# Optimization experiments

Measured on AMD Instinct MI355X. Metric: run time of the kernel, lower is better.

## Reference

```python
import jax, jax.numpy as jnp
import numpy as np

N = 100000   # nodes
E = 1600000  # edges
C = 128      # hidden_channels
L = 3        # num_layers
V = 128      # embedding vocab


def setup_inputs() -> dict:
    key = jax.random.key(0)
    ks = jax.random.split(key, 10)
    s = 1.0 / np.sqrt(C)
    return {
        "x_idx": jax.random.randint(ks[0], (N,), 0, V),
        "edge_index": jax.random.randint(ks[1], (2, E), 0, N),
        "edge_weight": jax.random.uniform(ks[2], (E,), dtype=jnp.float32),
        "emb": jax.random.normal(ks[3], (V, C), dtype=jnp.float32),
        "conv_w": jax.random.uniform(ks[4], (L, C, C), minval=-s, maxval=s, dtype=jnp.float32),
        "conv_b": jnp.zeros((L, C), dtype=jnp.float32),
        "lin1_w": jax.random.uniform(ks[5], (C, C), minval=-s, maxval=s, dtype=jnp.float32),
        "lin1_b": jnp.zeros((C,), dtype=jnp.float32),
        "lin2_w": jax.random.uniform(ks[6], (C, 2), minval=-s, maxval=s, dtype=jnp.float32),
        "lin2_b": jnp.zeros((2,), dtype=jnp.float32),
    }


def reference(x_idx, edge_index, edge_weight, emb, conv_w, conv_b,
              lin1_w, lin1_b, lin2_w, lin2_b):
    # GCNConv (PyG): add self-loops (weight 1), symmetric normalization
    row, col = edge_index[0], edge_index[1]
    loop = jnp.arange(N)
    r = jnp.concatenate([row, loop])
    c = jnp.concatenate([col, loop])
    w = jnp.concatenate([edge_weight, jnp.ones((N,), edge_weight.dtype)])
    deg = jax.ops.segment_sum(w, c, num_segments=N)            # [N]
    dinv = jnp.where(deg > 0, jax.lax.rsqrt(deg), 0.0)
    norm = dinv[r] * w * dinv[c]                               # [E+N]

    x = emb[x_idx]                                             # [N, C]
    for i in range(L):
        xw = x @ conv_w[i]                                     # [N, C]
        # message: norm * xw[src], aggregate at dst
        x = jax.ops.segment_sum(norm[:, None] * xw[r], c, num_segments=N) + conv_b[i]
        if i < L - 1:
            x = jax.nn.relu(x)  # dropout is identity in eval mode

    x = jax.nn.relu(x @ lin1_w + lin1_b)
    return x @ lin2_w + lin2_b                                 # [N, 2]
```

## Files before the change

kernel.cpp:

```cpp
#include <hip/hip_runtime.h>
#include <hip/hip_fp16.h>

#define NN 100000
#define NE 1600000
#define CC 128
#define NBIN 782
#define BPW 128
#define MAXB 2560
#define NHB 256
#define EPB 6250

typedef _Float16 f16x8 __attribute__((ext_vector_type(8)));
typedef float    f32x4 __attribute__((ext_vector_type(4)));

__global__ __launch_bounds__(256) void k_prep0(const int* __restrict__ ei,
                                               const float* __restrict__ conv_w,
                                               const float* __restrict__ lin1_w,
                                               const float* __restrict__ emb,
                                               int* __restrict__ hist,
                                               _Float16* __restrict__ wt,
                                               __half2* __restrict__ ewh,
                                               int* __restrict__ counter) {
    int blk = blockIdx.x;
    if (blk < NHB) {
        __shared__ int h[NBIN];
        for (int i = threadIdx.x; i < NBIN; i += 256) h[i] = 0;
        __syncthreads();
        int base = blk * EPB;
        for (int i = threadIdx.x; i < EPB; i += 256) {
            int d = ei[NE + base + i];
            atomicAdd(&h[d >> 7], 1);
        }
        __syncthreads();
        for (int i = threadIdx.x; i < NBIN; i += 256)
            hist[blk * NBIN + i] = h[i];
        if (blk == 0 && threadIdx.x == 0) *counter = 0;
    } else if (blk < NHB + 192) {
        int t = (blk - NHB) * 256 + threadIdx.x;
        int l = t >> 14, r = t & 16383;
        int j = r >> 7, k = r & 127;
        const float* src = (l < 2) ? (conv_w + (l + 1) * 16384) : lin1_w;
        wt[l * 16384 + j * 128 + k] = (_Float16)src[k * 128 + j];
    } else {
        int t = (blk - NHB - 192) * 256 + threadIdx.x;
        int i = t >> 6, jp = t & 63, j0 = jp * 2;
        float a0 = 0.f, a1 = 0.f;
        for (int k = 0; k < 128; k++) {
            float e = emb[i * 128 + k];
            a0 = fmaf(e, conv_w[k * 128 + j0], a0);
            a1 = fmaf(e, conv_w[k * 128 + j0 + 1], a1);
        }
        ewh[t] = __floats2half2_rn(a0, a1);
    }
}

__global__ __launch_bounds__(256) void k_scanA(const int* __restrict__ hist,
                                               int* __restrict__ blockBase,
                                               int* __restrict__ binTotal,
                                               int* __restrict__ binStart,
                                               int* __restrict__ counter) {
    __shared__ int s[256];
    __shared__ bool amLast;
    int bin = blockIdx.x, t = threadIdx.x;
    int v = hist[t * NBIN + bin];
    s[t] = v; __syncthreads();
    for (int off = 1; off < 256; off <<= 1) {
        int x = (t >= off) ? s[t - off] : 0;
        __syncthreads();
        s[t] += x;
        __syncthreads();
    }
    blockBase[t * NBIN + bin] = s[t] - v;
    if (t == 255) {
        binTotal[bin] = s[255];
        __threadfence();
        int d = atomicAdd(counter, 1);
        amLast = (d == NBIN - 1);
    }
    __syncthreads();
    if (!amLast) return;
    int loc[4];
    int sum = 0;
#pragma unroll
    for (int j = 0; j < 4; j++) {
        int idx = t * 4 + j;
        int x = (idx < NBIN) ? atomicAdd(&binTotal[idx], 0) : 0;
        loc[j] = sum; sum += x;
    }
    __syncthreads();
    s[t] = sum; __syncthreads();
    for (int off = 1; off < 256; off <<= 1) {
        int x = (t >= off) ? s[t - off] : 0;
        __syncthreads();
        s[t] += x;
        __syncthreads();
    }
    int base = s[t] - sum;
#pragma unroll
    for (int j = 0; j < 4; j++) {
        int idx = t * 4 + j;
        if (idx < NBIN) binStart[idx] = base + loc[j];
    }
    if (t == 255) binStart[NBIN] = s[255];
}

__global__ __launch_bounds__(256) void k_pass2(const int* __restrict__ ei,
                                               const float* __restrict__ ew,
                                               const int* __restrict__ binStart,
                                               const int* __restrict__ blockBase,
                                               int2* __restrict__ pay,
                                               unsigned char* __restrict__ key) {
    __shared__ int cur[NBIN];
    int blk = blockIdx.x;
    for (int i = threadIdx.x; i < NBIN; i += 256)
        cur[i] = binStart[i] + blockBase[blk * NBIN + i];
    __syncthreads();
    int base = blk * EPB;
    for (int i = threadIdx.x; i < EPB; i += 256) {
        int e = base + i;
        int d = ei[NE + e];
        int src = ei[e];
        float w = ew[e];
        int pos = atomicAdd(&cur[d >> 7], 1);
        pay[pos] = make_int2(src, __float_as_int(w));
        key[pos] = (unsigned char)(d & 127);
    }
}

__global__ __launch_bounds__(256) void k_pass3(const int* __restrict__ binStart,
                                               const int2* __restrict__ pay,
                                               const unsigned char* __restrict__ key,
                                               int2* __restrict__ csr,
                                               int* __restrict__ rowptr,
                                               float* __restrict__ dinv) {
    __shared__ int2 sp[MAXB];
    __shared__ unsigned char sk[MAXB];
    __shared__ int hist[BPW], excl[BPW], cur[BPW];
    __shared__ float degw[BPW];
    int b = blockIdx.x, t = threadIdx.x;
    int s0 = binStart[b], s1 = binStart[b + 1];
    int n = s1 - s0;
    if (t < BPW) { hist[t] = 0; degw[t] = 0.f; }
    __syncthreads();
    for (int i = t; i < n; i += 256) {
        int2 p = pay[s0 + i];
        unsigned char k = key[s0 + i];
        sp[i] = p; sk[i] = k;
        atomicAdd(&hist[k], 1);
    }
    __syncthreads();
    if (t < BPW) excl[t] = hist[t];
    __syncthreads();
    for (int off = 1; off < BPW; off <<= 1) {
        int x = (t < BPW && t >= off) ? excl[t - off] : 0;
        __syncthreads();
        if (t < BPW) excl[t] += x;
        __syncthreads();
    }
    if (t < BPW) {
        int ex = excl[t] - hist[t];
        excl[t] = ex;
        cur[t] = ex;
    }
    __syncthreads();
    int node0 = b * BPW;
    if (t < BPW && node0 + t < NN) rowptr[node0 + t] = s0 + excl[t];
    if (b == NBIN - 1 && t == 0) rowptr[NN] = NE;
    for (int i = t; i < n; i += 256) {
        int2 p = sp[i];
        unsigned char k = sk[i];
        int pos = atomicAdd(&cur[k], 1);
        csr[s0 + pos] = p;
        atomicAdd(&degw[k], __int_as_float(p.y));
    }
    __syncthreads();
    if (t < BPW && node0 + t < NN) dinv[node0 + t] = rsqrtf(1.f + degw[t]);
}

__global__ void k_mkcsr0(const int2* __restrict__ csr, const int* __restrict__ xidx,
                         const float* __restrict__ dinv, int2* __restrict__ csr0) {
    int e = blockIdx.x * 256 + threadIdx.x;
    if (e < NE) {
        int2 c = csr[e];
        csr0[e] = make_int2(xidx[c.x],
                            __float_as_int(__int_as_float(c.y) * dinv[c.x]));
    }
}

template <int SELF_TABLE, int RELU>
__device__ __forceinline__ void agg_core(const _Float16* __restrict__ src16,
                                         const int2* __restrict__ csr,
                                         const int* __restrict__ rowptr,
                                         const int* __restrict__ xidx,
                                         const float* __restrict__ dinv,
                                         const float* __restrict__ bias,
                                         _Float16* __restrict__ xout) {
    int wave = threadIdx.x >> 6, lane = threadIdx.x & 63;
    int g = lane >> 4, sub = lane & 15;
    int v = blockIdx.x * 4 + wave;
    if (v >= NN) return;
    int beg = rowptr[v], end = rowptr[v + 1];
    const unsigned long long* csr64 =
        reinterpret_cast<const unsigned long long*>(csr);

    auto lde = [&](int idx, float& w) -> f16x8 {
        unsigned long long raw = __builtin_nontemporal_load(csr64 + idx);
        int s = (int)(unsigned)(raw & 0xffffffffu);
        w = __int_as_float((int)(raw >> 32));
        return *reinterpret_cast<const f16x8*>(&src16[(size_t)s * 128 + sub * 8]);
    };

    float acc[8];
#pragma unroll
    for (int i = 0; i < 8; i++) acc[i] = 0.f;

    int e = beg;
    while (e + 16 <= end) {
        float w0, w1, w2, w3;
        f16x8 t0 = lde(e + g, w0);
        f16x8 t1 = lde(e + 4 + g, w1);
        f16x8 t2 = lde(e + 8 + g, w2);
        f16x8 t3 = lde(e + 12 + g, w3);
#pragma unroll
        for (int i = 0; i < 8; i++) acc[i] = fmaf(w0, (float)t0[i], acc[i]);
#pragma unroll
        for (int i = 0; i < 8; i++) acc[i] = fmaf(w1, (float)t1[i], acc[i]);
#pragma unroll
        for (int i = 0; i < 8; i++) acc[i] = fmaf(w2, (float)t2[i], acc[i]);
#pragma unroll
        for (int i = 0; i < 8; i++) acc[i] = fmaf(w3, (float)t3[i], acc[i]);
        e += 16;
    }
    if (e + 8 <= end) {
        float w0, w1;
        f16x8 t0 = lde(e + g, w0);
        f16x8 t1 = lde(e + 4 + g, w1);
#pragma unroll
        for (int i = 0; i < 8; i++) acc[i] = fmaf(w0, (float)t0[i], acc[i]);
#pragma unroll
        for (int i = 0; i < 8; i++) acc[i] = fmaf(w1, (float)t1[i], acc[i]);
        e += 8;
    }
    for (; e < end; e += 4) {
        int idx = e + g;
        bool ok = idx < end;
        float w0;
        f16x8 t0 = lde(ok ? idx : beg, w0);
        if (!ok) w0 = 0.f;
#pragma unroll
        for (int i = 0; i < 8; i++) acc[i] = fmaf(w0, (float)t0[i], acc[i]);
    }

#pragma unroll
    for (int i = 0; i < 8; i++) {
        acc[i] += __shfl_down(acc[i], 32);
        acc[i] += __shfl_down(acc[i], 16);
    }
    if (g == 0) {
        float dv = dinv[v];
        size_t selfoff = SELF_TABLE ? (size_t)xidx[v] * 128 : (size_t)v * 128;
        f16x8 sf = *reinterpret_cast<const f16x8*>(&src16[selfoff + sub * 8]);
        float4 b0 = reinterpret_cast<const float4*>(bias)[sub * 2];
        float4 b1 = reinterpret_cast<const float4*>(bias)[sub * 2 + 1];
        float bb[8] = {b0.x, b0.y, b0.z, b0.w, b1.x, b1.y, b1.z, b1.w};
        f16x8 o;
#pragma unroll
        for (int i = 0; i < 8; i++) {
            float self = SELF_TABLE ? dv * (float)sf[i] : (float)sf[i];
            float r = fmaf(dv, acc[i] + self, bb[i]);
            if (RELU) r = fmaxf(r, 0.f);
            o[i] = (_Float16)r;
        }
        __builtin_nontemporal_store(
            o, reinterpret_cast<f16x8*>(&xout[(size_t)v * 128 + sub * 8]));
    }
}

__global__ void k_agg0(const int2* __restrict__ csr0, const int* __restrict__ rowptr,
                       const int* __restrict__ xidx, const float* __restrict__ dinv,
                       const _Float16* __restrict__ ewh, const float* __restrict__ bias,
                       _Float16* __restrict__ xout) {
    agg_core<1, 1>(ewh, csr0, rowptr, xidx, dinv, bias, xout);
}

__global__ void k_agg_r(const _Float16* __restrict__ y, const int* __restrict__ rowptr,
                        const int2* __restrict__ csr, const float* __restrict__ dinv,
                        const float* __restrict__ bias, _Float16* __restrict__ xout) {
    agg_core<0, 1>(y, csr, rowptr, nullptr, dinv, bias, xout);
}

__global__ void k_agg_n(const _Float16* __restrict__ y, const int* __restrict__ rowptr,
                        const int2* __restrict__ csr, const float* __restrict__ dinv,
                        const float* __restrict__ bias, _Float16* __restrict__ xout) {
    agg_core<0, 0>(y, csr, rowptr, nullptr, dinv, bias, xout);
}

template <int MODE>
__global__ __launch_bounds__(256) void k_mgemm(const _Float16* __restrict__ A,
                                               const _Float16* __restrict__ Wt,
                                               const float* __restrict__ dinv,
                                               const float* __restrict__ bias,
                                               _Float16* __restrict__ yout,
                                               const float* __restrict__ w2,
                                               const float* __restrict__ b2,
                                               float* __restrict__ outf) {
    int wid = threadIdx.x >> 6, lane = threadIdx.x & 63;
    int lc = lane & 15, lg = lane >> 4;
    int arow = blockIdx.x * 64 + wid * 16 + lc;
    bool rok = arow < NN;

    f32x4 acc[8];
#pragma unroll
    for (int j = 0; j < 8; j++) acc[j] = (f32x4){0.f, 0.f, 0.f, 0.f};

#pragma unroll
    for (int kc = 0; kc < 4; kc++) {
        int k0 = kc * 32 + lg * 8;
        f16x8 a = {0, 0, 0, 0, 0, 0, 0, 0};
        if (rok) a = *reinterpret_cast<const f16x8*>(&A[arow * 128 + k0]);
#pragma unroll
        for (int j = 0; j < 8; j++) {
            f16x8 b = *reinterpret_cast<const f16x8*>(&Wt[(j * 16 + lc) * 128 + k0]);
            acc[j] = __builtin_amdgcn_mfma_f32_16x16x32_f16(a, b, acc[j], 0, 0, 0);
        }
    }

    int orow0 = blockIdx.x * 64 + wid * 16 + lg * 4;
    if (MODE == 0) {
        float dv[4];
#pragma unroll
        for (int r = 0; r < 4; r++)
            dv[r] = (orow0 + r < NN) ? dinv[orow0 + r] : 0.f;
#pragma unroll
        for (int j = 0; j < 8; j++) {
#pragma unroll
            for (int r = 0; r < 4; r++) {
                int orow = orow0 + r;
                if (orow < NN)
                    yout[orow * 128 + j * 16 + lc] = (_Float16)(dv[r] * acc[j][r]);
            }
        }
    } else {
        float bj[8], w0j[8], w1j[8];
#pragma unroll
        for (int j = 0; j < 8; j++) {
            int c = j * 16 + lc;
            bj[j] = bias[c];
            w0j[j] = w2[c * 2 + 0];
            w1j[j] = w2[c * 2 + 1];
        }
        float bb0 = b2[0], bb1 = b2[1];
#pragma unroll
        for (int r = 0; r < 4; r++) {
            float p0 = 0.f, p1 = 0.f;
#pragma unroll
            for (int j = 0; j < 8; j++) {
                float h = fmaxf(acc[j][r] + bj[j], 0.f);
                p0 = fmaf(h, w0j[j], p0);
                p1 = fmaf(h, w1j[j], p1);
            }
#pragma unroll
            for (int m = 1; m < 16; m <<= 1) {
                p0 += __shfl_xor(p0, m);
                p1 += __shfl_xor(p1, m);
            }
            int orow = orow0 + r;
            if (lc == 0 && orow < NN)
                *reinterpret_cast<float2*>(&outf[orow * 2]) =
                    make_float2(p0 + bb0, p1 + bb1);
        }
    }
}

extern "C" void kernel_launch(void* const* d_in, const int* in_sizes, int n_in,
                              void* d_out, int out_size, void* d_ws, size_t ws_size,
                              hipStream_t stream) {
    const int*   x_idx  = (const int*)d_in[0];
    const int*   ei     = (const int*)d_in[1];
    const float* ew     = (const float*)d_in[2];
    const float* emb    = (const float*)d_in[3];
    const float* conv_w = (const float*)d_in[4];
    const float* conv_b = (const float*)d_in[5];
    const float* lin1_w = (const float*)d_in[6];
    const float* lin1_b = (const float*)d_in[7];
    const float* lin2_w = (const float*)d_in[8];
    const float* lin2_b = (const float*)d_in[9];
    float* out = (float*)d_out;

    char* ws = (char*)d_ws;
    size_t off = 0;
    auto alloc = [&](size_t bytes) -> void* {
        void* p = ws + off;
        off += (bytes + 255) & ~(size_t)255;
        return p;
    };
    float*         dinv      = (float*)alloc(NN * 4);
    int*           rowptr    = (int*)alloc((NN + 1) * 4);
    int*           hist      = (int*)alloc((size_t)NHB * NBIN * 4);
    int*           blockBase = (int*)alloc((size_t)NHB * NBIN * 4);
    int*           binTotal  = (int*)alloc(NBIN * 4);
    int*           binStart  = (int*)alloc((NBIN + 1) * 4);
    int*           counter   = (int*)alloc(256);
    int2*          pay       = (int2*)alloc((size_t)NE * 8);
    unsigned char* key       = (unsigned char*)alloc(NE);
    int2*          csr       = (int2*)alloc((size_t)NE * 8);
    int2*          csr0      = (int2*)alloc((size_t)NE * 8);
    _Float16*      ewh       = (_Float16*)alloc(128 * 128 * 2);
    _Float16*      wt        = (_Float16*)alloc(3 * 128 * 128 * 2);
    _Float16*      xbuf      = (_Float16*)alloc((size_t)NN * CC * 2);
    _Float16*      ybuf      = (_Float16*)alloc((size_t)NN * CC * 2);
    (void)ws_size;

    const int NBe = (NE + 255) / 256;
    const int NBg = (NN + 63) / 64;

    k_prep0<<<NHB + 192 + 32, 256, 0, stream>>>(ei, conv_w, lin1_w, emb,
                                                hist, wt, (__half2*)ewh, counter);
    k_scanA<<<NBIN, 256, 0, stream>>>(hist, blockBase, binTotal, binStart, counter);
    k_pass2<<<NHB, 256, 0, stream>>>(ei, ew, binStart, blockBase, pay, key);
    k_pass3<<<NBIN, 256, 0, stream>>>(binStart, pay, key, csr, rowptr, dinv);
    k_mkcsr0<<<NBe, 256, 0, stream>>>(csr, x_idx, dinv, csr0);

    k_agg0<<<NN / 4, 256, 0, stream>>>(csr0, rowptr, x_idx, dinv, ewh,
                                       conv_b + 0 * CC, xbuf);
    k_mgemm<0><<<NBg, 256, 0, stream>>>(xbuf, wt + 0 * 16384, dinv, nullptr, ybuf,
                                        nullptr, nullptr, nullptr);
    k_agg_r<<<NN / 4, 256, 0, stream>>>(ybuf, rowptr, csr, dinv, conv_b + 1 * CC, xbuf);
    k_mgemm<0><<<NBg, 256, 0, stream>>>(xbuf, wt + 1 * 16384, dinv, nullptr, ybuf,
                                        nullptr, nullptr, nullptr);
    k_agg_n<<<NN / 4, 256, 0, stream>>>(ybuf, rowptr, csr, dinv, conv_b + 2 * CC, xbuf);
    k_mgemm<1><<<NBg, 256, 0, stream>>>(xbuf, wt + 2 * 16384, dinv, lin1_b, nullptr,
                                        lin2_w, lin2_b, out);
}
```

Baseline: 426.2 us.

## Fuse neighbor aggregation with following MFMA GEMM through shared memory

Merges each aggregation kernel with the following dense MFMA transform. Each block aggregates 64 nodes into an LDS tile, then multiplies that tile by the weights directly, so the intermediate x buffer never goes to global memory and three launches disappear. The trade-off is that each wave now walks 16 nodes one after another instead of one node per wave, with a grid about 16x smaller. The edge loop is also reduced from 16- to 8-edge unrolling with ordinary rather than nontemporal loads, which cuts memory-level parallelism in a gather-bound phase.

```diff
diff --git a/kernel.cpp b/kernel.cpp
--- a/kernel.cpp
+++ b/kernel.cpp
@@ -187,146 +187,98 @@
     }
 }
 
-template <int SELF_TABLE, int RELU>
-__device__ __forceinline__ void agg_core(const _Float16* __restrict__ src16,
-                                         const int2* __restrict__ csr,
-                                         const int* __restrict__ rowptr,
-                                         const int* __restrict__ xidx,
-                                         const float* __restrict__ dinv,
-                                         const float* __restrict__ bias,
-                                         _Float16* __restrict__ xout) {
-    int wave = threadIdx.x >> 6, lane = threadIdx.x & 63;
-    int g = lane >> 4, sub = lane & 15;
-    int v = blockIdx.x * 4 + wave;
-    if (v >= NN) return;
-    int beg = rowptr[v], end = rowptr[v + 1];
-    const unsigned long long* csr64 =
-        reinterpret_cast<const unsigned long long*>(csr);
-
-    auto lde = [&](int idx, float& w) -> f16x8 {
-        unsigned long long raw = __builtin_nontemporal_load(csr64 + idx);
-        int s = (int)(unsigned)(raw & 0xffffffffu);
-        w = __int_as_float((int)(raw >> 32));
-        return *reinterpret_cast<const f16x8*>(&src16[(size_t)s * 128 + sub * 8]);
-    };
-
-    float acc[8];
-#pragma unroll
-    for (int i = 0; i < 8; i++) acc[i] = 0.f;
-
-    int e = beg;
-    while (e + 16 <= end) {
-        float w0, w1, w2, w3;
-        f16x8 t0 = lde(e + g, w0);
-        f16x8 t1 = lde(e + 4 + g, w1);
-        f16x8 t2 = lde(e + 8 + g, w2);
-        f16x8 t3 = lde(e + 12 + g, w3);
-#pragma unroll
-        for (int i = 0; i < 8; i++) acc[i] = fmaf(w0, (float)t0[i], acc[i]);
-#pragma unroll
-        for (int i = 0; i < 8; i++) acc[i] = fmaf(w1, (float)t1[i], acc[i]);
-#pragma unroll
-        for (int i = 0; i < 8; i++) acc[i] = fmaf(w2, (float)t2[i], acc[i]);
-#pragma unroll
-        for (int i = 0; i < 8; i++) acc[i] = fmaf(w3, (float)t3[i], acc[i]);
-        e += 16;
-    }
-    if (e + 8 <= end) {
-        float w0, w1;
-        f16x8 t0 = lde(e + g, w0);
-        f16x8 t1 = lde(e + 4 + g, w1);
-#pragma unroll
-        for (int i = 0; i < 8; i++) acc[i] = fmaf(w0, (float)t0[i], acc[i]);
-#pragma unroll
-        for (int i = 0; i < 8; i++) acc[i] = fmaf(w1, (float)t1[i], acc[i]);
-        e += 8;
-    }
-    for (; e < end; e += 4) {
-        int idx = e + g;
-        bool ok = idx < end;
-        float w0;
-        f16x8 t0 = lde(ok ? idx : beg, w0);
-        if (!ok) w0 = 0.f;
-#pragma unroll
-        for (int i = 0; i < 8; i++) acc[i] = fmaf(w0, (float)t0[i], acc[i]);
-    }
-
-#pragma unroll
-    for (int i = 0; i < 8; i++) {
-        acc[i] += __shfl_down(acc[i], 32);
-        acc[i] += __shfl_down(acc[i], 16);
-    }
-    if (g == 0) {
-        float dv = dinv[v];
-        size_t selfoff = SELF_TABLE ? (size_t)xidx[v] * 128 : (size_t)v * 128;
-        f16x8 sf = *reinterpret_cast<const f16x8*>(&src16[selfoff + sub * 8]);
-        float4 b0 = reinterpret_cast<const float4*>(bias)[sub * 2];
-        float4 b1 = reinterpret_cast<const float4*>(bias)[sub * 2 + 1];
-        float bb[8] = {b0.x, b0.y, b0.z, b0.w, b1.x, b1.y, b1.z, b1.w};
-        f16x8 o;
-#pragma unroll
-        for (int i = 0; i < 8; i++) {
-            float self = SELF_TABLE ? dv * (float)sf[i] : (float)sf[i];
-            float r = fmaf(dv, acc[i] + self, bb[i]);
-            if (RELU) r = fmaxf(r, 0.f);
-            o[i] = (_Float16)r;
-        }
-        __builtin_nontemporal_store(
-            o, reinterpret_cast<f16x8*>(&xout[(size_t)v * 128 + sub * 8]));
-    }
-}
-
-__global__ void k_agg0(const int2* __restrict__ csr0, const int* __restrict__ rowptr,
-                       const int* __restrict__ xidx, const float* __restrict__ dinv,
-                       const _Float16* __restrict__ ewh, const float* __restrict__ bias,
-                       _Float16* __restrict__ xout) {
-    agg_core<1, 1>(ewh, csr0, rowptr, xidx, dinv, bias, xout);
-}
-
-__global__ void k_agg_r(const _Float16* __restrict__ y, const int* __restrict__ rowptr,
-                        const int2* __restrict__ csr, const float* __restrict__ dinv,
-                        const float* __restrict__ bias, _Float16* __restrict__ xout) {
-    agg_core<0, 1>(y, csr, rowptr, nullptr, dinv, bias, xout);
-}
-
-__global__ void k_agg_n(const _Float16* __restrict__ y, const int* __restrict__ rowptr,
-                        const int2* __restrict__ csr, const float* __restrict__ dinv,
-                        const float* __restrict__ bias, _Float16* __restrict__ xout) {
-    agg_core<0, 0>(y, csr, rowptr, nullptr, dinv, bias, xout);
-}
-
-template <int MODE>
-__global__ __launch_bounds__(256) void k_mgemm(const _Float16* __restrict__ A,
-                                               const _Float16* __restrict__ Wt,
+template <int SELF_TABLE, int RELU, int HEAD>
+__global__ __launch_bounds__(256) void k_fused(const _Float16* __restrict__ src16,
+                                               const int2* __restrict__ csr,
+                                               const int* __restrict__ rowptr,
+                                               const int* __restrict__ xidx,
                                                const float* __restrict__ dinv,
                                                const float* __restrict__ bias,
+                                               const _Float16* __restrict__ Wt,
                                                _Float16* __restrict__ yout,
+                                               const float* __restrict__ hb,
                                                const float* __restrict__ w2,
                                                const float* __restrict__ b2,
                                                float* __restrict__ outf) {
+    __shared__ _Float16 xs[64][136];
     int wid = threadIdx.x >> 6, lane = threadIdx.x & 63;
+    int g = lane >> 4, sub = lane & 15;
+    int nbase = blockIdx.x * 64 + wid * 16;
+
+    for (int n = 0; n < 16; n++) {
+        int v = nbase + n;
+        if (v >= NN) break;
+        int beg = rowptr[v], end = rowptr[v + 1];
+        float acc[8];
+#pragma unroll
+        for (int i = 0; i < 8; i++) acc[i] = 0.f;
+        int e = beg;
+        while (e + 8 <= end) {
+            int2 c0 = csr[e + g];
+            int2 c1 = csr[e + 4 + g];
+            f16x8 t0 =
+                *reinterpret_cast<const f16x8*>(&src16[(size_t)c0.x * 128 + sub * 8]);
+            f16x8 t1 =
+                *reinterpret_cast<const f16x8*>(&src16[(size_t)c1.x * 128 + sub * 8]);
+            float w0 = __int_as_float(c0.y), w1 = __int_as_float(c1.y);
+#pragma unroll
+            for (int i = 0; i < 8; i++) acc[i] = fmaf(w0, (float)t0[i], acc[i]);
+#pragma unroll
+            for (int i = 0; i < 8; i++) acc[i] = fmaf(w1, (float)t1[i], acc[i]);
+            e += 8;
+        }
+        for (; e < end; e += 4) {
+            int idx = e + g;
+            bool ok = idx < end;
+            int2 c0 = csr[ok ? idx : beg];
+            float w0 = ok ? __int_as_float(c0.y) : 0.f;
+            f16x8 t0 =
+                *reinterpret_cast<const f16x8*>(&src16[(size_t)c0.x * 128 + sub * 8]);
+#pragma unroll
+            for (int i = 0; i < 8; i++) acc[i] = fmaf(w0, (float)t0[i], acc[i]);
+        }
+#pragma unroll
+        for (int i = 0; i < 8; i++) {
+            acc[i] += __shfl_down(acc[i], 32);
+            acc[i] += __shfl_down(acc[i], 16);
+        }
+        if (g == 0) {
+            float dv = dinv[v];
+            size_t selfoff = SELF_TABLE ? (size_t)xidx[v] * 128 : (size_t)v * 128;
+            f16x8 sf = *reinterpret_cast<const f16x8*>(&src16[selfoff + sub * 8]);
+            float4 b0 = reinterpret_cast<const float4*>(bias)[sub * 2];
+            float4 b1 = reinterpret_cast<const float4*>(bias)[sub * 2 + 1];
+            float bb[8] = {b0.x, b0.y, b0.z, b0.w, b1.x, b1.y, b1.z, b1.w};
+            f16x8 o;
+#pragma unroll
+            for (int i = 0; i < 8; i++) {
+                float self = SELF_TABLE ? dv * (float)sf[i] : (float)sf[i];
+                float r = fmaf(dv, acc[i] + self, bb[i]);
+                if (RELU) r = fmaxf(r, 0.f);
+                o[i] = (_Float16)r;
+            }
+            *reinterpret_cast<f16x8*>(&xs[wid * 16 + n][sub * 8]) = o;
+        }
+    }
+    __syncthreads();
+
     int lc = lane & 15, lg = lane >> 4;
-    int arow = blockIdx.x * 64 + wid * 16 + lc;
-    bool rok = arow < NN;
-
-    f32x4 acc[8];
-#pragma unroll
-    for (int j = 0; j < 8; j++) acc[j] = (f32x4){0.f, 0.f, 0.f, 0.f};
-
+    f32x4 acc2[8];
+#pragma unroll
+    for (int j = 0; j < 8; j++) acc2[j] = (f32x4){0.f, 0.f, 0.f, 0.f};
 #pragma unroll
     for (int kc = 0; kc < 4; kc++) {
         int k0 = kc * 32 + lg * 8;
-        f16x8 a = {0, 0, 0, 0, 0, 0, 0, 0};
-        if (rok) a = *reinterpret_cast<const f16x8*>(&A[arow * 128 + k0]);
+        f16x8 a = *reinterpret_cast<const f16x8*>(&xs[wid * 16 + lc][k0]);
 #pragma unroll
         for (int j = 0; j < 8; j++) {
             f16x8 b = *reinterpret_cast<const f16x8*>(&Wt[(j * 16 + lc) * 128 + k0]);
-            acc[j] = __builtin_amdgcn_mfma_f32_16x16x32_f16(a, b, acc[j], 0, 0, 0);
+            acc2[j] = __builtin_amdgcn_mfma_f32_16x16x32_f16(a, b, acc2[j], 0, 0, 0);
         }
     }
 
     int orow0 = blockIdx.x * 64 + wid * 16 + lg * 4;
-    if (MODE == 0) {
+    if (HEAD == 0) {
         float dv[4];
 #pragma unroll
         for (int r = 0; r < 4; r++)
@@ -337,7 +289,8 @@
             for (int r = 0; r < 4; r++) {
                 int orow = orow0 + r;
                 if (orow < NN)
-                    yout[orow * 128 + j * 16 + lc] = (_Float16)(dv[r] * acc[j][r]);
+                    yout[(size_t)orow * 128 + j * 16 + lc] =
+                        (_Float16)(dv[r] * acc2[j][r]);
             }
         }
     } else {
@@ -345,7 +298,7 @@
 #pragma unroll
         for (int j = 0; j < 8; j++) {
             int c = j * 16 + lc;
-            bj[j] = bias[c];
+            bj[j] = hb[c];
             w0j[j] = w2[c * 2 + 0];
             w1j[j] = w2[c * 2 + 1];
         }
@@ -355,7 +308,7 @@
             float p0 = 0.f, p1 = 0.f;
 #pragma unroll
             for (int j = 0; j < 8; j++) {
-                float h = fmaxf(acc[j][r] + bj[j], 0.f);
+                float h = fmaxf(acc2[j][r] + bj[j], 0.f);
                 p0 = fmaf(h, w0j[j], p0);
                 p1 = fmaf(h, w1j[j], p1);
             }
@@ -407,8 +360,8 @@
     int2*          csr0      = (int2*)alloc((size_t)NE * 8);
     _Float16*      ewh       = (_Float16*)alloc(128 * 128 * 2);
     _Float16*      wt        = (_Float16*)alloc(3 * 128 * 128 * 2);
-    _Float16*      xbuf      = (_Float16*)alloc((size_t)NN * CC * 2);
-    _Float16*      ybuf      = (_Float16*)alloc((size_t)NN * CC * 2);
+    _Float16*      ybufA     = (_Float16*)alloc((size_t)NN * CC * 2);
+    _Float16*      ybufB     = (_Float16*)alloc((size_t)NN * CC * 2);
     (void)ws_size;
 
     const int NBe = (NE + 255) / 256;
@@ -421,14 +374,13 @@
     k_pass3<<<NBIN, 256, 0, stream>>>(binStart, pay, key, csr, rowptr, dinv);
     k_mkcsr0<<<NBe, 256, 0, stream>>>(csr, x_idx, dinv, csr0);
 
-    k_agg0<<<NN / 4, 256, 0, stream>>>(csr0, rowptr, x_idx, dinv, ewh,
-                                       conv_b + 0 * CC, xbuf);
-    k_mgemm<0><<<NBg, 256, 0, stream>>>(xbuf, wt + 0 * 16384, dinv, nullptr, ybuf,
-                                        nullptr, nullptr, nullptr);
-    k_agg_r<<<NN / 4, 256, 0, stream>>>(ybuf, rowptr, csr, dinv, conv_b + 1 * CC, xbuf);
-    k_mgemm<0><<<NBg, 256, 0, stream>>>(xbuf, wt + 1 * 16384, dinv, nullptr, ybuf,
-                                        nullptr, nullptr, nullptr);
-    k_agg_n<<<NN / 4, 256, 0, stream>>>(ybuf, rowptr, csr, dinv, conv_b + 2 * CC, xbuf);
-    k_mgemm<1><<<NBg, 256, 0, stream>>>(xbuf, wt + 2 * 16384, dinv, lin1_b, nullptr,
-                                        lin2_w, lin2_b, out);
-}
+    k_fused<1, 1, 0><<<NBg, 256, 0, stream>>>(ewh, csr0, rowptr, x_idx, dinv,
+                                              conv_b + 0 * CC, wt + 0 * 16384, ybufA,
+                                              nullptr, nullptr, nullptr, nullptr);
+    k_fused<0, 1, 0><<<NBg, 256, 0, stream>>>(ybufA, csr, rowptr, nullptr, dinv,
+                                              conv_b + 1 * CC, wt + 1 * 16384, ybufB,
+                                              nullptr, nullptr, nullptr, nullptr);
+    k_fused<0, 0, 1><<<NBg, 256, 0, stream>>>(ybufB, csr, rowptr, nullptr, dinv,
+                                              conv_b + 2 * CC, wt + 2 * 16384, nullptr,
+                                              lin1_b, lin2_w, lin2_b, out);
+}
```

New measurement: 486.0 us. 1.14x slower.
